# Performance work log

Hardware: AMD Instinct MI355X
Metric: run time of the kernel (lower is better)

Reference implementation:

```python
import jax, jax.numpy as jnp
import numpy as np


def setup_inputs() -> dict:
    key = jax.random.key(0)
    k1, k2, k3, k4, k5 = jax.random.split(key, 5)
    B, F, E, NF = 16384, 1024, 64, 32
    return {
        "input": jax.random.normal(k1, (B, F), dtype=jnp.float32),
        "fields": jax.random.randint(k2, (F,), 0, NF, dtype=jnp.int32),
        "w_weight": jax.random.normal(k3, (1, F), dtype=jnp.float32) * 0.02,
        "w_bias": jax.random.normal(k4, (1,), dtype=jnp.float32) * 0.02,
        "vs": jax.random.normal(k5, (NF, F, E), dtype=jnp.float32) * 0.05,
    }


def reference(input, fields, w_weight, w_bias, vs):
    # Linear (1st-order) term: [B, 1]
    linear = input @ w_weight.T + w_bias

    F = input.shape[1]
    # Gather field-aware embedding tables per feature: G[k, i, e] = vs[fields[k], i, e]
    G = vs[fields]  # [F, F, E]
    # A[i, j] = dot(vs[fields[j], i, :], vs[fields[i], j, :])
    A = jnp.einsum("jie,ije->ij", G, G)  # [F, F]
    # P[i, j] = sum_b input[b, i] * input[b, j]  (original sums over batch)
    P = input.T @ input  # [F, F]
    # second_order = sum_{i < j} A[i, j] * P[i, j]  (scalar, as in the source)
    second_order = jnp.sum(jnp.triu(A * P, k=1))

    return jax.nn.sigmoid(linear + second_order)
```

## Files before the change

kernel.cpp:

```cpp
#include <hip/hip_runtime.h>
#include <hip/hip_fp16.h>
#include <math.h>
#include <stdint.h>

#define FDIM 1024
#define BTOT 16384
#define EDIM 64
#define NFLD 32
#define NPANEL 4
#define NPAIRS 10

typedef _Float16 half8 __attribute__((ext_vector_type(8)));
typedef __fp16 fp16x2 __attribute__((ext_vector_type(2)));
typedef float f32x4 __attribute__((ext_vector_type(4)));

__device__ __forceinline__ uint32_t pk2(float a, float b){
  fp16x2 h = __builtin_amdgcn_cvt_pkrtz(a, b);
  return __builtin_bit_cast(uint32_t, h);
}

__device__ __forceinline__ void gload16(const void* g, void* l){
  __builtin_amdgcn_global_load_lds((const __attribute__((address_space(1))) void*)g,
                                   (__attribute__((address_space(3))) void*)l,
                                   16, 0, 0);
}

__device__ __forceinline__ float fget(const float4& v, int i){
  switch (i){ case 0: return v.x; case 1: return v.y; case 2: return v.z; default: return v.w; }
}

__device__ __forceinline__ int pairId(int ti, int tj){
  return ti * NPANEL - (ti * (ti + 1)) / 2 + tj;
}

__global__ __launch_bounds__(256, 4) void mid_fused(
    const float* __restrict__ vs, const int* __restrict__ fields,
    _Float16* __restrict__ Wp,
    const float* __restrict__ X, const float* __restrict__ w,
    uint4* __restrict__ Xbt, float* __restrict__ linp){
  const int t = threadIdx.x;

  if (blockIdx.x < 2048){
    const int bx = blockIdx.x;
    const int p  = bx & 3;
    const int kb = bx >> 2;
    const int ro = t >> 6;
    const int l  = t & 63;
    const int og = kb * 4 + ro;
    const int k0 = og * 8;
    const int c0 = p * 256;

    float4 rv[8];
#pragma unroll
    for (int r = 0; r < 8; ++r)
      rv[r] = *(const float4*)(X + (size_t)(k0 + r) * FDIM + c0 + 4 * l);

    const float4 w4 = *(const float4*)(w + c0 + 4 * l);
#pragma unroll
    for (int r = 0; r < 8; ++r){
      float lp = rv[r].x * w4.x + rv[r].y * w4.y + rv[r].z * w4.z + rv[r].w * w4.w;
#pragma unroll
      for (int off = 32; off; off >>= 1) lp += __shfl_xor(lp, off, 64);
      if (l == 0) linp[(size_t)p * BTOT + k0 + r] = lp;
    }

    uint4* dst = Xbt + ((size_t)p * 2048 + og) * 256;
#pragma unroll
    for (int i = 0; i < 4; ++i){
      uint4 ch;
      ch.x = pk2(fget(rv[0], i), fget(rv[1], i));
      ch.y = pk2(fget(rv[2], i), fget(rv[3], i));
      ch.z = pk2(fget(rv[4], i), fget(rv[5], i));
      ch.w = pk2(fget(rv[6], i), fget(rv[7], i));
      dst[4 * l + i] = ch;
    }
    return;
  }

  __shared__ float Si[32][68];
  __shared__ float Sj[32][68];
  __shared__ int gI[32], gJ[32];
  __shared__ int cnt[NFLD], pos[NFLD], off[NFLD + 1];
  __shared__ int permS[FDIM];

  if (t < NFLD) cnt[t] = 0;
  __syncthreads();
#pragma unroll
  for (int r = 0; r < 4; ++r) atomicAdd(&cnt[fields[t + 256 * r]], 1);
  __syncthreads();
  if (t == 0){
    int s = 0;
    for (int i = 0; i < NFLD; ++i){ off[i] = s; s += cnt[i]; }
    off[NFLD] = s;
  }
  __syncthreads();
  if (t < NFLD) pos[t] = off[t];
  __syncthreads();
#pragma unroll
  for (int r = 0; r < 4; ++r){
    const int idx = t + 256 * r;
    const int p = atomicAdd(&pos[fields[idx]], 1);
    permS[p] = idx;
  }
  __syncthreads();

  const int a = (blockIdx.x - 2048) >> 5, b = (blockIdx.x - 2048) & 31;
  const int oa = off[a], na = off[a + 1] - oa;
  const int ob = off[b], nb_ = off[b + 1] - ob;
  if (na == 0 || nb_ == 0) return;
  for (int ia0 = 0; ia0 < na; ia0 += 32){
    const int nac = min(32, na - ia0);
    for (int jb0 = 0; jb0 < nb_; jb0 += 32){
      const int nbc = min(32, nb_ - jb0);
      __syncthreads();
      if (t < 32){
        gI[t] = (t < nac) ? permS[oa + ia0 + t] : 0;
        gJ[t] = (t < nbc) ? permS[ob + jb0 + t] : 0;
      }
      __syncthreads();
#pragma unroll
      for (int rep = 0; rep < 2; ++rep){
        const int lidx = rep * 256 + t;
        const int r = lidx >> 4, e4 = (lidx & 15) * 4;
        if (r < nac)
          *(float4*)&Si[r][e4] = *(const float4*)(vs + ((size_t)b * FDIM + gI[r]) * EDIM + e4);
        if (r < nbc)
          *(float4*)&Sj[r][e4] = *(const float4*)(vs + ((size_t)a * FDIM + gJ[r]) * EDIM + e4);
      }
      __syncthreads();
      const int jr = t & 31;
      const int ir0 = t >> 5;
      for (int ko = 0; ko * 8 < nac; ++ko){
        const int ir = ko * 8 + ir0;
        if (ir < nac && jr < nbc){
          float dot = 0.f;
#pragma unroll
          for (int e4 = 0; e4 < EDIM; e4 += 4){
            const float4 x = *(const float4*)&Si[ir][e4];
            const float4 y = *(const float4*)&Sj[jr][e4];
            dot += x.x * y.x + x.y * y.y + x.z * y.z + x.w * y.w;
          }
          const int gi = gI[ir], gj = gJ[jr];
          const int pi = gi >> 8, pj = gj >> 8;
          if (pi <= pj){
            const float v = (gj > gi) ? dot : 0.f;
            const int li = gi & 255, lj = gj & 255;
            const int P  = pairId(pi, pj);
            const int w8 = (li >> 7) * 4 + (lj >> 6);
            const int mb = (li >> 4) & 7, r_ = li & 3;
            const int lane = ((li >> 2) & 3) * 16 + (lj & 15);
            const int nbv = (lj >> 4) & 3;
            const size_t o_ = (size_t)(P * 8 + w8) * 8192
                            + (size_t)((mb * 2 + (r_ >> 1)) * 64 + lane) * 8
                            + (r_ & 1) * 4 + nbv;
            Wp[o_] = (_Float16)v;
          }
        }
      }
    }
  }
}

__global__ __launch_bounds__(512, 1) void gram_kc(
    const uint4* __restrict__ Xbt, const _Float16* __restrict__ Wp,
    float* __restrict__ partial){
  __shared__ uint4 lds4[8192];
  const int t = threadIdx.x, w = t >> 6, lane = t & 63;
  const int orow = lane >> 4, rl = lane & 15;
  const int wr = w >> 2, wc = w & 3;
  const int b8 = blockIdx.x * 8;

#pragma unroll
  for (int p = 0; p < NPANEL; ++p)
#pragma unroll
    for (int q = 0; q < 4; ++q){
      const int m = q * 512 + t;
      const int o = m >> 8, c = m & 255;
      gload16(Xbt + ((size_t)p * 2048 + b8 + o) * 256 + c,
              lds4 + o * 1024 + p * 256 + c);
    }

  float wsum = 0.f;

  auto loadB = [&](int tj, half8 (&bf)[2][4]){
#pragma unroll
    for (int s = 0; s < 2; ++s)
#pragma unroll
      for (int nb = 0; nb < 4; ++nb)
        bf[s][nb] = __builtin_bit_cast(half8,
            lds4[(s * 4 + orow) * 1024 + tj * 256 + wc * 64 + nb * 16 + rl]);
  };

  auto body = [&](int ti, int tj, const half8 (&bf)[2][4]){
    if (ti == tj && wr == 1 && wc < 2) return;

    const uint4* wp = (const uint4*)(Wp + (size_t)(pairId(ti, tj) * 8 + w) * 8192);
    half8 wreg[16];
#pragma unroll
    for (int q = 0; q < 16; ++q)
      wreg[q] = __builtin_bit_cast(half8, wp[q * 64 + lane]);

    f32x4 acc[8][4];
#pragma unroll
    for (int i = 0; i < 8; ++i)
#pragma unroll
      for (int j = 0; j < 4; ++j) acc[i][j] = {0.f, 0.f, 0.f, 0.f};
#pragma unroll
    for (int s = 0; s < 2; ++s)
#pragma unroll
      for (int mb = 0; mb < 8; ++mb){
        const half8 af = __builtin_bit_cast(half8,
            lds4[(s * 4 + orow) * 1024 + ti * 256 + wr * 128 + mb * 16 + rl]);
#pragma unroll
        for (int nb = 0; nb < 4; ++nb)
          acc[mb][nb] = __builtin_amdgcn_mfma_f32_16x16x32_f16(
              af, bf[s][nb], acc[mb][nb], 0, 0, 0);
      }
#pragma unroll
    for (int mb = 0; mb < 8; ++mb)
#pragma unroll
      for (int h = 0; h < 2; ++h){
        const half8 hv = wreg[mb * 2 + h];
#pragma unroll
        for (int r2 = 0; r2 < 2; ++r2)
#pragma unroll
          for (int nb = 0; nb < 4; ++nb)
            wsum += (float)hv[r2 * 4 + nb] * acc[mb][nb][2 * h + r2];
      }
  };

#define GRAM_GROUP(G, VM)                                         \
  asm volatile("s_waitcnt vmcnt(" #VM ")" ::: "memory");          \
  __builtin_amdgcn_s_barrier();                                   \
  {                                                               \
    half8 bf[2][4];                                               \
    loadB(G, bf);                                                 \
    _Pragma("unroll 1")                                           \
    for (int ti = 0; ti <= (G); ++ti) body(ti, (G), bf);          \
  }

  GRAM_GROUP(0, 12)
  GRAM_GROUP(1, 8)
  GRAM_GROUP(2, 4)
  GRAM_GROUP(3, 0)
#undef GRAM_GROUP

#pragma unroll
  for (int off = 32; off; off >>= 1) wsum += __shfl_xor(wsum, off, 64);
  __syncthreads();
  float* red = (float*)lds4;
  if (lane == 0) red[w] = wsum;
  __syncthreads();
  if (t == 0){
    float s = 0.f;
#pragma unroll
    for (int i = 0; i < 8; ++i) s += red[i];
    partial[blockIdx.x] = s;
  }
}

__global__ __launch_bounds__(256) void final_out(
    const float* __restrict__ partial, const float* __restrict__ linp,
    const float* __restrict__ wb, float* __restrict__ out){
  __shared__ float red[256];
  const int t = threadIdx.x;
  red[t] = partial[t];
  __syncthreads();
  for (int off = 128; off; off >>= 1){
    if (t < off) red[t] += red[t + off];
    __syncthreads();
  }
  const float stot = red[0] + wb[0];
  const int i = blockIdx.x * 256 + t;
  float z = stot;
#pragma unroll
  for (int p = 0; p < NPANEL; ++p) z += linp[(size_t)p * BTOT + i];
  out[i] = 1.f / (1.f + expf(-z));
}

extern "C" void kernel_launch(void* const* d_in, const int* in_sizes, int n_in,
                              void* d_out, int out_size, void* d_ws,
                              size_t ws_size, hipStream_t stream) {
  const float* X      = (const float*)d_in[0];
  const int* fields   = (const int*)d_in[1];
  const float* ww     = (const float*)d_in[2];
  const float* wbias  = (const float*)d_in[3];
  const float* vs     = (const float*)d_in[4];
  float* out          = (float*)d_out;

  char* ws = (char*)d_ws;
  float* partial = (float*)ws;
  float* linp = (float*)(ws + (64 << 10));
  _Float16* Wp = (_Float16*)(ws + (size_t)(4 << 20));
  uint4* Xbt = (uint4*)(ws + (size_t)(8 << 20));


  mid_fused<<<2048 + 1024, 256, 0, stream>>>(vs, fields, Wp, X, ww, Xbt, linp);
  gram_kc<<<256, 512, 0, stream>>>(Xbt, Wp, partial);
  final_out<<<BTOT / 256, 256, 0, stream>>>(partial, linp, wbias, out);
}
```

Measured before the change: 68.33 us.

## Fuse fp32-to-fp16 X conversion and linear term into gram kernel with pipelined loads

Drops the separate pass that converted X to a packed fp16 transposed buffer in global memory. Each gram block now reads its fp32 rows directly, computes the linear dot product, and packs the data into swizzled LDS. Loads for later panels overlap MFMA work on earlier ones. This removes a global write and re-read of X and lets the W-table kernel run alone. In exchange, the gram kernel has a longer critical path with more register pressure, and the MFMA body is split into halves to cut accumulator registers.

```diff
diff --git a/kernel.cpp b/kernel.cpp
--- a/kernel.cpp
+++ b/kernel.cpp
@@ -19,12 +19,6 @@
   return __builtin_bit_cast(uint32_t, h);
 }
 
-__device__ __forceinline__ void gload16(const void* g, void* l){
-  __builtin_amdgcn_global_load_lds((const __attribute__((address_space(1))) void*)g,
-                                   (__attribute__((address_space(3))) void*)l,
-                                   16, 0, 0);
-}
-
 __device__ __forceinline__ float fget(const float4& v, int i){
   switch (i){ case 0: return v.x; case 1: return v.y; case 2: return v.z; default: return v.w; }
 }
@@ -33,55 +27,17 @@
   return ti * NPANEL - (ti * (ti + 1)) / 2 + tj;
 }
 
-__global__ __launch_bounds__(256, 4) void mid_fused(
+#define SWZ(c) ((c) ^ (((c) >> 3) & 7))
+
+__global__ __launch_bounds__(256) void w2_kernel(
     const float* __restrict__ vs, const int* __restrict__ fields,
-    _Float16* __restrict__ Wp,
-    const float* __restrict__ X, const float* __restrict__ w,
-    uint4* __restrict__ Xbt, float* __restrict__ linp){
-  const int t = threadIdx.x;
-
-  if (blockIdx.x < 2048){
-    const int bx = blockIdx.x;
-    const int p  = bx & 3;
-    const int kb = bx >> 2;
-    const int ro = t >> 6;
-    const int l  = t & 63;
-    const int og = kb * 4 + ro;
-    const int k0 = og * 8;
-    const int c0 = p * 256;
-
-    float4 rv[8];
-#pragma unroll
-    for (int r = 0; r < 8; ++r)
-      rv[r] = *(const float4*)(X + (size_t)(k0 + r) * FDIM + c0 + 4 * l);
-
-    const float4 w4 = *(const float4*)(w + c0 + 4 * l);
-#pragma unroll
-    for (int r = 0; r < 8; ++r){
-      float lp = rv[r].x * w4.x + rv[r].y * w4.y + rv[r].z * w4.z + rv[r].w * w4.w;
-#pragma unroll
-      for (int off = 32; off; off >>= 1) lp += __shfl_xor(lp, off, 64);
-      if (l == 0) linp[(size_t)p * BTOT + k0 + r] = lp;
-    }
-
-    uint4* dst = Xbt + ((size_t)p * 2048 + og) * 256;
-#pragma unroll
-    for (int i = 0; i < 4; ++i){
-      uint4 ch;
-      ch.x = pk2(fget(rv[0], i), fget(rv[1], i));
-      ch.y = pk2(fget(rv[2], i), fget(rv[3], i));
-      ch.z = pk2(fget(rv[4], i), fget(rv[5], i));
-      ch.w = pk2(fget(rv[6], i), fget(rv[7], i));
-      dst[4 * l + i] = ch;
-    }
-    return;
-  }
-
+    _Float16* __restrict__ Wp){
   __shared__ float Si[32][68];
   __shared__ float Sj[32][68];
   __shared__ int gI[32], gJ[32];
   __shared__ int cnt[NFLD], pos[NFLD], off[NFLD + 1];
   __shared__ int permS[FDIM];
+  const int t = threadIdx.x;
 
   if (t < NFLD) cnt[t] = 0;
   __syncthreads();
@@ -104,7 +60,7 @@
   }
   __syncthreads();
 
-  const int a = (blockIdx.x - 2048) >> 5, b = (blockIdx.x - 2048) & 31;
+  const int a = blockIdx.x >> 5, b = blockIdx.x & 31;
   const int oa = off[a], na = off[a + 1] - oa;
   const int ob = off[b], nb_ = off[b + 1] - ob;
   if (na == 0 || nb_ == 0) return;
@@ -161,24 +117,59 @@
   }
 }
 
-__global__ __launch_bounds__(512, 1) void gram_kc(
-    const uint4* __restrict__ Xbt, const _Float16* __restrict__ Wp,
-    float* __restrict__ partial){
+__global__ __launch_bounds__(512, 1) void gram_fused(
+    const float* __restrict__ X, const float* __restrict__ w,
+    const _Float16* __restrict__ Wp,
+    float* __restrict__ partial, float* __restrict__ lin){
   __shared__ uint4 lds4[8192];
-  const int t = threadIdx.x, w = t >> 6, lane = t & 63;
+  const int t = threadIdx.x, wv = t >> 6, lane = t & 63;
   const int orow = lane >> 4, rl = lane & 15;
-  const int wr = w >> 2, wc = w & 3;
-  const int b8 = blockIdx.x * 8;
-
-#pragma unroll
-  for (int p = 0; p < NPANEL; ++p)
-#pragma unroll
-    for (int q = 0; q < 4; ++q){
-      const int m = q * 512 + t;
-      const int o = m >> 8, c = m & 255;
-      gload16(Xbt + ((size_t)p * 2048 + b8 + o) * 256 + c,
-              lds4 + o * 1024 + p * 256 + c);
-    }
+  const int wr = wv >> 2, wc = wv & 3;
+  const int k0 = blockIdx.x * 64 + wv * 8;
+
+  int swA[8], swB[4];
+#pragma unroll
+  for (int mb = 0; mb < 8; ++mb){ const int c = wr * 128 + mb * 16 + rl; swA[mb] = SWZ(c); }
+#pragma unroll
+  for (int nb = 0; nb < 4; ++nb){ const int c = wc * 64 + nb * 16 + rl; swB[nb] = SWZ(c); }
+
+  float4 w4[4];
+#pragma unroll
+  for (int p = 0; p < 4; ++p) w4[p] = *(const float4*)(w + p * 256 + 4 * lane);
+
+  float lp[8];
+#pragma unroll
+  for (int r = 0; r < 8; ++r) lp[r] = 0.f;
+
+  float4 rvA[8], rvB[8];
+
+#define ISSUE(rv, p)                                                          \
+  _Pragma("unroll")                                                           \
+  for (int r = 0; r < 8; ++r)                                                 \
+    rv[r] = *(const float4*)(X + (size_t)(k0 + r) * FDIM + (p) * 256 + 4 * lane);
+
+#define PROCESS(rv, p)                                                        \
+  {                                                                           \
+    _Pragma("unroll")                                                         \
+    for (int r = 0; r < 8; ++r)                                               \
+      lp[r] += rv[r].x * w4[p].x + rv[r].y * w4[p].y                          \
+             + rv[r].z * w4[p].z + rv[r].w * w4[p].w;                         \
+    uint4* base_ = lds4 + wv * 1024 + (p) * 256;                              \
+    _Pragma("unroll")                                                         \
+    for (int i = 0; i < 4; ++i){                                              \
+      uint4 ch;                              \
+      ch.x = pk2(fget(rv[0], i), fget(rv[1], i));                             \
+      ch.y = pk2(fget(rv[2], i), fget(rv[3], i));                             \
+      ch.z = pk2(fget(rv[4], i), fget(rv[5], i));                             \
+      ch.w = pk2(fget(rv[6], i), fget(rv[7], i));                             \
+      base_[SWZ(4 * lane + i)] = ch;                                          \
+    }                                                                         \
+  }
+
+#define BARRIER                                                               \
+  asm volatile("s_waitcnt lgkmcnt(0)" ::: "memory");                          \
+  __builtin_amdgcn_s_barrier();                                               \
+  asm volatile("" ::: "memory");
 
   float wsum = 0.f;
 
@@ -188,50 +179,52 @@
 #pragma unroll
       for (int nb = 0; nb < 4; ++nb)
         bf[s][nb] = __builtin_bit_cast(half8,
-            lds4[(s * 4 + orow) * 1024 + tj * 256 + wc * 64 + nb * 16 + rl]);
+            lds4[(s * 4 + orow) * 1024 + tj * 256 + swB[nb]]);
+  };
+
+  auto half_body = [&](int ti, int tj, int mb0, const half8 (&bf)[2][4]){
+    const uint4* wp = (const uint4*)(Wp + (size_t)(pairId(ti, tj) * 8 + wv) * 8192);
+    half8 wreg[8];
+#pragma unroll
+    for (int q = 0; q < 8; ++q)
+      wreg[q] = __builtin_bit_cast(half8, wp[(mb0 * 2 + q) * 64 + lane]);
+
+    f32x4 acc[4][4];
+#pragma unroll
+    for (int i = 0; i < 4; ++i)
+#pragma unroll
+      for (int j = 0; j < 4; ++j) acc[i][j] = {0.f, 0.f, 0.f, 0.f};
+#pragma unroll
+    for (int s = 0; s < 2; ++s)
+#pragma unroll
+      for (int m = 0; m < 4; ++m){
+        const half8 af = __builtin_bit_cast(half8,
+            lds4[(s * 4 + orow) * 1024 + ti * 256 + swA[mb0 + m]]);
+#pragma unroll
+        for (int nb = 0; nb < 4; ++nb)
+          acc[m][nb] = __builtin_amdgcn_mfma_f32_16x16x32_f16(
+              af, bf[s][nb], acc[m][nb], 0, 0, 0);
+      }
+#pragma unroll
+    for (int m = 0; m < 4; ++m)
+#pragma unroll
+      for (int h = 0; h < 2; ++h){
+        const half8 hv = wreg[m * 2 + h];
+#pragma unroll
+        for (int r2 = 0; r2 < 2; ++r2)
+#pragma unroll
+          for (int nb = 0; nb < 4; ++nb)
+            wsum += (float)hv[r2 * 4 + nb] * acc[m][nb][2 * h + r2];
+      }
   };
 
   auto body = [&](int ti, int tj, const half8 (&bf)[2][4]){
     if (ti == tj && wr == 1 && wc < 2) return;
-
-    const uint4* wp = (const uint4*)(Wp + (size_t)(pairId(ti, tj) * 8 + w) * 8192);
-    half8 wreg[16];
-#pragma unroll
-    for (int q = 0; q < 16; ++q)
-      wreg[q] = __builtin_bit_cast(half8, wp[q * 64 + lane]);
-
-    f32x4 acc[8][4];
-#pragma unroll
-    for (int i = 0; i < 8; ++i)
-#pragma unroll
-      for (int j = 0; j < 4; ++j) acc[i][j] = {0.f, 0.f, 0.f, 0.f};
-#pragma unroll
-    for (int s = 0; s < 2; ++s)
-#pragma unroll
-      for (int mb = 0; mb < 8; ++mb){
-        const half8 af = __builtin_bit_cast(half8,
-            lds4[(s * 4 + orow) * 1024 + ti * 256 + wr * 128 + mb * 16 + rl]);
-#pragma unroll
-        for (int nb = 0; nb < 4; ++nb)
-          acc[mb][nb] = __builtin_amdgcn_mfma_f32_16x16x32_f16(
-              af, bf[s][nb], acc[mb][nb], 0, 0, 0);
-      }
-#pragma unroll
-    for (int mb = 0; mb < 8; ++mb)
-#pragma unroll
-      for (int h = 0; h < 2; ++h){
-        const half8 hv = wreg[mb * 2 + h];
-#pragma unroll
-        for (int r2 = 0; r2 < 2; ++r2)
-#pragma unroll
-          for (int nb = 0; nb < 4; ++nb)
-            wsum += (float)hv[r2 * 4 + nb] * acc[mb][nb][2 * h + r2];
-      }
+    half_body(ti, tj, 0, bf);
+    half_body(ti, tj, 4, bf);
   };
 
-#define GRAM_GROUP(G, VM)                                         \
-  asm volatile("s_waitcnt vmcnt(" #VM ")" ::: "memory");          \
-  __builtin_amdgcn_s_barrier();                                   \
+#define GROUP(G)                                                  \
   {                                                               \
     half8 bf[2][4];                                               \
     loadB(G, bf);                                                 \
@@ -239,17 +232,35 @@
     for (int ti = 0; ti <= (G); ++ti) body(ti, (G), bf);          \
   }
 
-  GRAM_GROUP(0, 12)
-  GRAM_GROUP(1, 8)
-  GRAM_GROUP(2, 4)
-  GRAM_GROUP(3, 0)
-#undef GRAM_GROUP
+  ISSUE(rvA, 0); ISSUE(rvB, 1);
+  PROCESS(rvA, 0);
+  ISSUE(rvA, 2);
+  BARRIER; GROUP(0);
+  PROCESS(rvB, 1);
+  ISSUE(rvB, 3);
+  BARRIER; GROUP(1);
+  PROCESS(rvA, 2);
+  BARRIER; GROUP(2);
+  PROCESS(rvB, 3);
+#pragma unroll
+  for (int r = 0; r < 8; ++r){
+    float v = lp[r];
+#pragma unroll
+    for (int off = 32; off; off >>= 1) v += __shfl_xor(v, off, 64);
+    if (lane == 0) lin[k0 + r] = v;
+  }
+  BARRIER; GROUP(3);
+
+#undef GROUP
+#undef BARRIER
+#undef PROCESS
+#undef ISSUE
 
 #pragma unroll
   for (int off = 32; off; off >>= 1) wsum += __shfl_xor(wsum, off, 64);
   __syncthreads();
   float* red = (float*)lds4;
-  if (lane == 0) red[w] = wsum;
+  if (lane == 0) red[wv] = wsum;
   __syncthreads();
   if (t == 0){
     float s = 0.f;
@@ -260,7 +271,7 @@
 }
 
 __global__ __launch_bounds__(256) void final_out(
-    const float* __restrict__ partial, const float* __restrict__ linp,
+    const float* __restrict__ partial, const float* __restrict__ lin,
     const float* __restrict__ wb, float* __restrict__ out){
   __shared__ float red[256];
   const int t = threadIdx.x;
@@ -272,9 +283,7 @@
   }
   const float stot = red[0] + wb[0];
   const int i = blockIdx.x * 256 + t;
-  float z = stot;
-#pragma unroll
-  for (int p = 0; p < NPANEL; ++p) z += linp[(size_t)p * BTOT + i];
+  const float z = lin[i] + stot;
   out[i] = 1.f / (1.f + expf(-z));
 }
 
@@ -290,12 +299,11 @@
 
   char* ws = (char*)d_ws;
   float* partial = (float*)ws;
-  float* linp = (float*)(ws + (64 << 10));
+  float* lin = (float*)(ws + (64 << 10));
   _Float16* Wp = (_Float16*)(ws + (size_t)(4 << 20));
-  uint4* Xbt = (uint4*)(ws + (size_t)(8 << 20));
-
-
-  mid_fused<<<2048 + 1024, 256, 0, stream>>>(vs, fields, Wp, X, ww, Xbt, linp);
-  gram_kc<<<256, 512, 0, stream>>>(Xbt, Wp, partial);
-  final_out<<<BTOT / 256, 256, 0, stream>>>(partial, linp, wbias, out);
-}
+
+
+  w2_kernel<<<NFLD * NFLD, 256, 0, stream>>>(vs, fields, Wp);
+  gram_fused<<<256, 512, 0, stream>>>(X, ww, Wp, partial, lin);
+  final_out<<<BTOT / 256, 256, 0, stream>>>(partial, lin, wbias, out);
+}
```

Measured after the change: 88.22 us. 29.1% more time.
